# Optimization experiments

Measured on AMD Instinct MI355X. Metric: run time of the kernel, lower is better.

Reference implementation:

```python
import jax, jax.numpy as jnp
import numpy as np

TEMPERATURE = 0.07


def setup_inputs() -> dict:
    key = jax.random.key(0)
    k1, k2 = jax.random.split(key)
    image_tokens = jax.random.normal(k1, (128, 196, 512), dtype=jnp.float32)
    text_tokens = jax.random.normal(k2, (128, 64, 512), dtype=jnp.float32)
    return {"image_tokens": image_tokens, "text_tokens": text_tokens}


def _maxsim(image_tokens, text_tokens):
    # sim[b1, b2, t, i] = <text[b1, t], image[b2, i]>
    sim = jnp.einsum('btd,sid->bsti', text_tokens, image_tokens)  # [B, B, T, I]
    sim_max = jnp.max(sim, axis=-1)        # max over image tokens -> [B, B, T]
    return jnp.mean(sim_max, axis=-1)      # mean over text tokens -> [B, B]


def _cross_entropy_diag(logits):
    # CE against targets = arange(B): mean(logsumexp(row) - row[b, b])
    lse = jax.nn.logsumexp(logits, axis=-1)
    diag = jnp.diagonal(logits)
    return jnp.mean(lse - diag)


def reference(image_tokens, text_tokens):
    sim = _maxsim(image_tokens, text_tokens)
    logits = sim / TEMPERATURE
    loss_i2t = _cross_entropy_diag(logits)
    loss_t2i = _cross_entropy_diag(logits.T)
    return (loss_i2t + loss_t2i) * 0.5
```

## Files before the change

### kernel.cpp

```cpp
#include <hip/hip_runtime.h>
#include <stdint.h>


typedef __attribute__((ext_vector_type(4))) int i4v;

#define BB 128
#define TT 64
#define II 196
#define IP 208
#define DD 512
#define BKK 64
#define KSTEPS (DD / BKK)

static __device__ __forceinline__ void async16(const void* g, void* l) {
  __builtin_amdgcn_global_load_lds(
      (const __attribute__((address_space(1))) void*)g,
      (__attribute__((address_space(3))) void*)l, 16, 0, 0);
}

static __device__ __forceinline__ unsigned q8(float x) {
  float r = rintf(x * 32.0f);
  r = fmaxf(-127.0f, fminf(127.0f, r));
  return (unsigned)((int)r) & 255u;
}

static __device__ __forceinline__ unsigned pk4(float a, float b, float c, float d) {
  return q8(a) | (q8(b) << 8) | (q8(c) << 16) | (q8(d) << 24);
}

#define TEXT_BLOCKS 1024
#define IMG_BLOCKS  3328
__global__ void pack_k(const float* __restrict__ img, const float* __restrict__ txt,
                       uint4* __restrict__ imgq, uint4* __restrict__ txtq) {
  uint4 o;
  if (blockIdx.x < TEXT_BLOCKS) {
    int c = blockIdx.x * 256 + threadIdx.x;
    const float4* in4 = (const float4*)txt;
    float4 f0 = in4[4 * c], f1 = in4[4 * c + 1], f2 = in4[4 * c + 2], f3 = in4[4 * c + 3];
    o.x = pk4(f0.x, f0.y, f0.z, f0.w);
    o.y = pk4(f1.x, f1.y, f1.z, f1.w);
    o.z = pk4(f2.x, f2.y, f2.z, f2.w);
    o.w = pk4(f3.x, f3.y, f3.z, f3.w);
    txtq[c] = o;
  } else {
    int c = (blockIdx.x - TEXT_BLOCKS) * 256 + threadIdx.x;
    int e = c * 16;
    int k = e & (DD - 1);
    int tok = e >> 9;
    int b2 = tok / IP;
    int r = tok - b2 * IP;
    if (r < II) {
      const float4* in4 = (const float4*)(img + ((size_t)(b2 * II + r) * DD + k));
      float4 f0 = in4[0], f1 = in4[1], f2 = in4[2], f3 = in4[3];
      o.x = pk4(f0.x, f0.y, f0.z, f0.w);
      o.y = pk4(f1.x, f1.y, f1.z, f1.w);
      o.z = pk4(f2.x, f2.y, f2.z, f2.w);
      o.w = pk4(f3.x, f3.y, f3.z, f3.w);
    } else {
      o = make_uint4(0u, 0u, 0u, 0u);
    }
    imgq[c] = o;
  }
}

__global__ __launch_bounds__(256, 2) void maxsim_gemm_k(
    const char* __restrict__ A,
    const char* __restrict__ Bm,
    float* __restrict__ sim)
{
  __shared__ __align__(16) char As0[128 * BKK], As1[128 * BKK];
  __shared__ __align__(16) char Bs0[IP * BKK],  Bs1[IP * BKK];
  __shared__ int partial[2][128];

  const int pr  = blockIdx.x;
  const int b2  = blockIdx.y;
  const int tid = threadIdx.x;
  const int w = tid >> 6, l = tid & 63;
  const int m = l & 15, q = l >> 4;
  const int waveM = w >> 1;
  const int waveN = w & 1;
  const int nt = 7 - waveN;

  const int ca0 = tid, ca1 = tid + 256;
  const int cb0 = tid, cb1 = tid + 256, cb2 = tid + 512, cb3 = 768 + l;
#define AOFF(c) ((unsigned)((pr * 128 + ((c) >> 2)) * DD + ((((c) & 3) ^ ((((c) >> 2) >> 1) & 3)) * 16)))
#define BOFF(c) ((unsigned)((b2 * IP + ((c) >> 2)) * DD + ((((c) & 3) ^ ((((c) >> 2) >> 1) & 3)) * 16)))
  const unsigned oA0 = AOFF(ca0), oA1 = AOFF(ca1);
  const unsigned oB0 = BOFF(cb0), oB1 = BOFF(cb1), oB2 = BOFF(cb2), oB3 = BOFF(cb3);

#define ISSUE(AS, BS, k0) do {                                    \
    async16(A  + oA0 + (k0), (char*)(AS) + ca0 * 16);             \
    async16(A  + oA1 + (k0), (char*)(AS) + ca1 * 16);             \
    async16(Bm + oB0 + (k0), (char*)(BS) + cb0 * 16);             \
    async16(Bm + oB1 + (k0), (char*)(BS) + cb1 * 16);             \
    async16(Bm + oB2 + (k0), (char*)(BS) + cb2 * 16);             \
    if (w == 0) async16(Bm + oB3 + (k0), (char*)(BS) + cb3 * 16); \
  } while (0)

  i4v acc[4][7];
#pragma unroll
  for (int mi = 0; mi < 4; ++mi)
#pragma unroll
    for (int nj = 0; nj < 7; ++nj)
      acc[mi][nj] = (i4v){0, 0, 0, 0};

  const int swz = q ^ ((m >> 1) & 3);

#define COMPUTE(AS, BS) do {                                               \
    const i4v* Av = (const i4v*)(AS);                                      \
    const i4v* Bv = (const i4v*)(BS);                                      \
    i4v af[4];                                                             \
    _Pragma("unroll")                                                      \
    for (int mi = 0; mi < 4; ++mi)                                         \
      af[mi] = Av[(waveM * 64 + mi * 16 + m) * 4 + swz];                   \
    _Pragma("unroll")                                                      \
    for (int nj = 0; nj < 7; ++nj) {                                       \
      if (nj < nt) {                                                       \
        i4v bf = Bv[(waveN * 112 + nj * 16 + m) * 4 + swz];                \
        _Pragma("unroll")                                                  \
        for (int mi = 0; mi < 4; ++mi)                                     \
          acc[mi][nj] = __builtin_amdgcn_mfma_i32_16x16x64_i8(             \
              af[mi], bf, acc[mi][nj], 0, 0, 0);                           \
      }                                                                    \
    }                                                                      \
  } while (0)

  ISSUE(As0, Bs0, 0);
  __syncthreads();
  for (int ks = 0; ks < KSTEPS; ks += 2) {
    ISSUE(As1, Bs1, (ks + 1) * BKK);
    COMPUTE(As0, Bs0);
    __syncthreads();
    if (ks + 2 < KSTEPS) ISSUE(As0, Bs0, (ks + 2) * BKK);
    COMPUTE(As1, Bs1);
    __syncthreads();
  }

  const int NEG = -(1 << 30);
#pragma unroll
  for (int mi = 0; mi < 4; ++mi) {
    int v0 = NEG, v1 = NEG, v2 = NEG, v3 = NEG;
#pragma unroll
    for (int nj = 0; nj < 7; ++nj) {
      if (nj < nt) {
        int col = waveN * 112 + nj * 16 + m;
        bool valid = col < II;
        v0 = max(v0, valid ? acc[mi][nj][0] : NEG);
        v1 = max(v1, valid ? acc[mi][nj][1] : NEG);
        v2 = max(v2, valid ? acc[mi][nj][2] : NEG);
        v3 = max(v3, valid ? acc[mi][nj][3] : NEG);
      }
    }
#pragma unroll
    for (int off = 1; off < 16; off <<= 1) {
      v0 = max(v0, __shfl_xor(v0, off));
      v1 = max(v1, __shfl_xor(v1, off));
      v2 = max(v2, __shfl_xor(v2, off));
      v3 = max(v3, __shfl_xor(v3, off));
    }
    if (m == 0) {
      int rowb = waveM * 64 + mi * 16 + q * 4;
      partial[waveN][rowb + 0] = v0;
      partial[waveN][rowb + 1] = v1;
      partial[waveN][rowb + 2] = v2;
      partial[waveN][rowb + 3] = v3;
    }
  }
  __syncthreads();

  if (tid < 128) {
    int v = max(partial[0][tid], partial[1][tid]);
#pragma unroll
    for (int off = 1; off < 64; off <<= 1) v += __shfl_xor(v, off);
    if ((tid & 63) == 0) {
      int b1 = pr * 2 + (tid >> 6);
      sim[b1 * BB + b2] = (float)v * (1.0f / 65536.0f);
    }
  }
}

#define LSTR 132
__global__ void loss_k(const float* __restrict__ sim, float* __restrict__ out) {
  __shared__ float S[BB * LSTR];
  __shared__ float red[4];
  const int tid = threadIdx.x;
#pragma unroll
  for (int i = 0; i < 16; ++i) {
    int c = tid + 256 * i;
    int r = c >> 5, col4 = c & 31;
    float4 v = ((const float4*)sim)[c];
    *(float4*)&S[r * LSTR + col4 * 4] = v;
  }
  __syncthreads();

  const int b = tid & 127;
  const bool rowmode = tid < 128;
  const float sc = 1.0f / 0.07f;
  float mx = -3.0e38f;
  for (int j = 0; j < BB; ++j) {
    float v = rowmode ? S[b * LSTR + j] : S[j * LSTR + b];
    mx = fmaxf(mx, v);
  }
  float s = 0.f;
  for (int j = 0; j < BB; ++j) {
    float v = rowmode ? S[b * LSTR + j] : S[j * LSTR + b];
    s += __expf((v - mx) * sc);
  }
  float d = S[b * LSTR + b];
  float v = (mx - d) * sc + __logf(s);
#pragma unroll
  for (int off = 1; off < 64; off <<= 1) v += __shfl_xor(v, off);
  if ((tid & 63) == 0) red[tid >> 6] = v;
  __syncthreads();
  if (tid == 0) out[0] = (red[0] + red[1] + red[2] + red[3]) * 0.5f / 128.0f;
}

extern "C" void kernel_launch(void* const* d_in, const int* in_sizes, int n_in,
                              void* d_out, int out_size, void* d_ws, size_t ws_size,
                              hipStream_t stream) {
  const float* img = (const float*)d_in[0];
  const float* txt = (const float*)d_in[1];
  float* out = (float*)d_out;

  char* ws = (char*)d_ws;
  const size_t TXT_Q = (size_t)BB * TT * DD;
  const size_t IMG_Q = (size_t)BB * IP * DD;
  char* txtq = ws;
  char* imgq = ws + TXT_Q;
  float* sim = (float*)(ws + TXT_Q + IMG_Q);

  pack_k<<<TEXT_BLOCKS + IMG_BLOCKS, 256, 0, stream>>>(img, txt, (uint4*)imgq, (uint4*)txtq);
  maxsim_gemm_k<<<dim3(64, 128), 256, 0, stream>>>(txtq, imgq, sim);
  loss_k<<<1, 256, 0, stream>>>(sim, out);
}
```

Before: 227.7 us.

## Make GEMM persistent over image batches and fuse loss via last-block counter

Each of 512 blocks now loops over 16 image batches for a fixed text tile. The next batch's first K-slice is prefetched while the current batch finishes, so the tile pipeline carries across batches instead of restarting per block. The MFMA work is rebalanced so the 13th N-tile is split between the two waves and no padded-column tiles are computed. The separate loss kernel is folded in: the last block, found through an atomic counter, does the loss, at the cost of an extra memset and threadfences.

```diff
diff --git a/kernel.cpp b/kernel.cpp
--- a/kernel.cpp
+++ b/kernel.cpp
@@ -10,7 +10,8 @@
 #define IP 208
 #define DD 512
 #define BKK 64
-#define KSTEPS (DD / BKK)
+#define NTASK 16
+#define LSTR 132
 
 static __device__ __forceinline__ void async16(const void* g, void* l) {
   __builtin_amdgcn_global_load_lds(
@@ -23,7 +24,6 @@
   r = fmaxf(-127.0f, fminf(127.0f, r));
   return (unsigned)((int)r) & 255u;
 }
-
 static __device__ __forceinline__ unsigned pk4(float a, float b, float c, float d) {
   return q8(a) | (q8(b) << 8) | (q8(c) << 16) | (q8(d) << 24);
 }
@@ -66,43 +66,53 @@
 __global__ __launch_bounds__(256, 2) void maxsim_gemm_k(
     const char* __restrict__ A,
     const char* __restrict__ Bm,
-    float* __restrict__ sim)
+    float* __restrict__ sim,
+    int* __restrict__ counter,
+    float* __restrict__ out)
 {
-  __shared__ __align__(16) char As0[128 * BKK], As1[128 * BKK];
-  __shared__ __align__(16) char Bs0[IP * BKK],  Bs1[IP * BKK];
-  __shared__ int partial[2][128];
-
-  const int pr  = blockIdx.x;
-  const int b2  = blockIdx.y;
+  __shared__ __align__(16) char smem[BB * LSTR * 4];
+  char* As0 = smem;
+  char* As1 = smem + 8192;
+  char* Bs0 = smem + 16384;
+  char* Bs1 = smem + 29696;
+  int*  partial = (int*)(smem + 43008);
+  __shared__ float red[4];
+  __shared__ int lastflag;
+
+  const int j   = blockIdx.x;
+  const int pr  = j >> 3;
+  const int b2_0 = j & 7;
   const int tid = threadIdx.x;
   const int w = tid >> 6, l = tid & 63;
   const int m = l & 15, q = l >> 4;
   const int waveM = w >> 1;
   const int waveN = w & 1;
-  const int nt = 7 - waveN;
 
   const int ca0 = tid, ca1 = tid + 256;
   const int cb0 = tid, cb1 = tid + 256, cb2 = tid + 512, cb3 = 768 + l;
 #define AOFF(c) ((unsigned)((pr * 128 + ((c) >> 2)) * DD + ((((c) & 3) ^ ((((c) >> 2) >> 1) & 3)) * 16)))
-#define BOFF(c) ((unsigned)((b2 * IP + ((c) >> 2)) * DD + ((((c) & 3) ^ ((((c) >> 2) >> 1) & 3)) * 16)))
+#define BOFF(c) ((unsigned)((b2_0 * IP + ((c) >> 2)) * DD + ((((c) & 3) ^ ((((c) >> 2) >> 1) & 3)) * 16)))
   const unsigned oA0 = AOFF(ca0), oA1 = AOFF(ca1);
   const unsigned oB0 = BOFF(cb0), oB1 = BOFF(cb1), oB2 = BOFF(cb2), oB3 = BOFF(cb3);
-
-#define ISSUE(AS, BS, k0) do {                                    \
-    async16(A  + oA0 + (k0), (char*)(AS) + ca0 * 16);             \
-    async16(A  + oA1 + (k0), (char*)(AS) + ca1 * 16);             \
-    async16(Bm + oB0 + (k0), (char*)(BS) + cb0 * 16);             \
-    async16(Bm + oB1 + (k0), (char*)(BS) + cb1 * 16);             \
-    async16(Bm + oB2 + (k0), (char*)(BS) + cb2 * 16);             \
-    if (w == 0) async16(Bm + oB3 + (k0), (char*)(BS) + cb3 * 16); \
+  const unsigned BSTR = 8u * IP * DD;
+
+#define ISSUE(AS, BS, k0, bo_) do {                                      \
+    async16(A  + oA0 + (k0), (AS) + ca0 * 16);                           \
+    async16(A  + oA1 + (k0), (AS) + ca1 * 16);                           \
+    async16(Bm + oB0 + (bo_) + (k0), (BS) + cb0 * 16);                   \
+    async16(Bm + oB1 + (bo_) + (k0), (BS) + cb1 * 16);                   \
+    async16(Bm + oB2 + (bo_) + (k0), (BS) + cb2 * 16);                   \
+    if (w == 0) async16(Bm + oB3 + (bo_) + (k0), (BS) + cb3 * 16);       \
   } while (0)
 
-  i4v acc[4][7];
+  i4v am[4][6], a12[2];
 #pragma unroll
   for (int mi = 0; mi < 4; ++mi)
 #pragma unroll
-    for (int nj = 0; nj < 7; ++nj)
-      acc[mi][nj] = (i4v){0, 0, 0, 0};
+    for (int nj = 0; nj < 6; ++nj)
+      am[mi][nj] = (i4v){0, 0, 0, 0};
+  a12[0] = (i4v){0, 0, 0, 0};
+  a12[1] = (i4v){0, 0, 0, 0};
 
   const int swz = q ^ ((m >> 1) & 3);
 
@@ -114,76 +124,105 @@
     for (int mi = 0; mi < 4; ++mi)                                         \
       af[mi] = Av[(waveM * 64 + mi * 16 + m) * 4 + swz];                   \
     _Pragma("unroll")                                                      \
-    for (int nj = 0; nj < 7; ++nj) {                                       \
-      if (nj < nt) {                                                       \
-        i4v bf = Bv[(waveN * 112 + nj * 16 + m) * 4 + swz];                \
-        _Pragma("unroll")                                                  \
-        for (int mi = 0; mi < 4; ++mi)                                     \
-          acc[mi][nj] = __builtin_amdgcn_mfma_i32_16x16x64_i8(             \
-              af[mi], bf, acc[mi][nj], 0, 0, 0);                           \
+    for (int nj = 0; nj < 6; ++nj) {                                       \
+      i4v bf = Bv[((waveN * 6 + nj) * 16 + m) * 4 + swz];                  \
+      _Pragma("unroll")                                                    \
+      for (int mi = 0; mi < 4; ++mi)                                       \
+        am[mi][nj] = __builtin_amdgcn_mfma_i32_16x16x64_i8(                \
+            af[mi], bf, am[mi][nj], 0, 0, 0);                              \
+    }                                                                      \
+    {                                                                      \
+      i4v bf = Bv[(192 + m) * 4 + swz];                                    \
+      if (waveN == 0) {                                                    \
+        a12[0] = __builtin_amdgcn_mfma_i32_16x16x64_i8(af[0], bf, a12[0], 0, 0, 0); \
+        a12[1] = __builtin_amdgcn_mfma_i32_16x16x64_i8(af[1], bf, a12[1], 0, 0, 0); \
+      } else {                                                             \
+        a12[0] = __builtin_amdgcn_mfma_i32_16x16x64_i8(af[2], bf, a12[0], 0, 0, 0); \
+        a12[1] = __builtin_amdgcn_mfma_i32_16x16x64_i8(af[3], bf, a12[1], 0, 0, 0); \
       }                                                                    \
     }                                                                      \
   } while (0)
 
-  ISSUE(As0, Bs0, 0);
-  __syncthreads();
-  for (int ks = 0; ks < KSTEPS; ks += 2) {
-    ISSUE(As1, Bs1, (ks + 1) * BKK);
-    COMPUTE(As0, Bs0);
+  unsigned bo = 0;
+  ISSUE(As0, Bs0, 0, 0);
+  __syncthreads();
+
+#pragma unroll 1
+  for (int t = 0; t < NTASK; ++t) {
+    for (int ks = 0; ks < 8; ks += 2) {
+      ISSUE(As1, Bs1, (ks + 1) * BKK, bo);
+      COMPUTE(As0, Bs0);
+      __syncthreads();
+      if (ks + 2 < 8)            ISSUE(As0, Bs0, (ks + 2) * BKK, bo);
+      else if (t + 1 < NTASK)    ISSUE(As0, Bs0, 0, bo + BSTR);
+      COMPUTE(As1, Bs1);
+      __syncthreads();
+    }
+
+    const int NEG = -(1 << 30);
+#pragma unroll
+    for (int mi = 0; mi < 4; ++mi) {
+      int v0 = NEG, v1 = NEG, v2 = NEG, v3 = NEG;
+#pragma unroll
+      for (int nj = 0; nj < 6; ++nj) {
+        v0 = max(v0, am[mi][nj][0]);
+        v1 = max(v1, am[mi][nj][1]);
+        v2 = max(v2, am[mi][nj][2]);
+        v3 = max(v3, am[mi][nj][3]);
+      }
+      if ((mi >> 1) == waveN) {
+        int z = mi & 1;
+        bool valid = m < 4;
+        v0 = max(v0, valid ? a12[z][0] : NEG);
+        v1 = max(v1, valid ? a12[z][1] : NEG);
+        v2 = max(v2, valid ? a12[z][2] : NEG);
+        v3 = max(v3, valid ? a12[z][3] : NEG);
+      }
+#pragma unroll
+      for (int off = 1; off < 16; off <<= 1) {
+        v0 = max(v0, __shfl_xor(v0, off));
+        v1 = max(v1, __shfl_xor(v1, off));
+        v2 = max(v2, __shfl_xor(v2, off));
+        v3 = max(v3, __shfl_xor(v3, off));
+      }
+      if (m == 0) {
+        int rowb = waveM * 64 + mi * 16 + q * 4;
+        partial[waveN * 128 + rowb + 0] = v0;
+        partial[waveN * 128 + rowb + 1] = v1;
+        partial[waveN * 128 + rowb + 2] = v2;
+        partial[waveN * 128 + rowb + 3] = v3;
+      }
+    }
     __syncthreads();
-    if (ks + 2 < KSTEPS) ISSUE(As0, Bs0, (ks + 2) * BKK);
-    COMPUTE(As1, Bs1);
+
+    if (tid < 128) {
+      int v = max(partial[tid], partial[128 + tid]);
+#pragma unroll
+      for (int off = 1; off < 64; off <<= 1) v += __shfl_xor(v, off);
+      if ((tid & 63) == 0) {
+        int b1 = pr * 2 + (tid >> 6);
+        sim[b1 * BB + (b2_0 + 8 * t)] = (float)v * (1.0f / 65536.0f);
+      }
+    }
     __syncthreads();
-  }
-
-  const int NEG = -(1 << 30);
-#pragma unroll
-  for (int mi = 0; mi < 4; ++mi) {
-    int v0 = NEG, v1 = NEG, v2 = NEG, v3 = NEG;
-#pragma unroll
-    for (int nj = 0; nj < 7; ++nj) {
-      if (nj < nt) {
-        int col = waveN * 112 + nj * 16 + m;
-        bool valid = col < II;
-        v0 = max(v0, valid ? acc[mi][nj][0] : NEG);
-        v1 = max(v1, valid ? acc[mi][nj][1] : NEG);
-        v2 = max(v2, valid ? acc[mi][nj][2] : NEG);
-        v3 = max(v3, valid ? acc[mi][nj][3] : NEG);
-      }
-    }
-#pragma unroll
-    for (int off = 1; off < 16; off <<= 1) {
-      v0 = max(v0, __shfl_xor(v0, off));
-      v1 = max(v1, __shfl_xor(v1, off));
-      v2 = max(v2, __shfl_xor(v2, off));
-      v3 = max(v3, __shfl_xor(v3, off));
-    }
-    if (m == 0) {
-      int rowb = waveM * 64 + mi * 16 + q * 4;
-      partial[waveN][rowb + 0] = v0;
-      partial[waveN][rowb + 1] = v1;
-      partial[waveN][rowb + 2] = v2;
-      partial[waveN][rowb + 3] = v3;
-    }
-  }
-  __syncthreads();
-
-  if (tid < 128) {
-    int v = max(partial[0][tid], partial[1][tid]);
-#pragma unroll
-    for (int off = 1; off < 64; off <<= 1) v += __shfl_xor(v, off);
-    if ((tid & 63) == 0) {
-      int b1 = pr * 2 + (tid >> 6);
-      sim[b1 * BB + b2] = (float)v * (1.0f / 65536.0f);
-    }
-  }
-}
-
-#define LSTR 132
-__global__ void loss_k(const float* __restrict__ sim, float* __restrict__ out) {
-  __shared__ float S[BB * LSTR];
-  __shared__ float red[4];
-  const int tid = threadIdx.x;
+
+#pragma unroll
+    for (int mi = 0; mi < 4; ++mi)
+#pragma unroll
+      for (int nj = 0; nj < 6; ++nj)
+        am[mi][nj] = (i4v){0, 0, 0, 0};
+    a12[0] = (i4v){0, 0, 0, 0};
+    a12[1] = (i4v){0, 0, 0, 0};
+    bo += BSTR;
+  }
+
+  __threadfence();
+  if (tid == 0) lastflag = (atomicAdd(counter, 1) == 511);
+  __syncthreads();
+  if (!lastflag) return;
+  __threadfence();
+
+  float* S = (float*)smem;
 #pragma unroll
   for (int i = 0; i < 16; ++i) {
     int c = tid + 256 * i;
@@ -197,13 +236,13 @@
   const bool rowmode = tid < 128;
   const float sc = 1.0f / 0.07f;
   float mx = -3.0e38f;
-  for (int j = 0; j < BB; ++j) {
-    float v = rowmode ? S[b * LSTR + j] : S[j * LSTR + b];
+  for (int jj = 0; jj < BB; ++jj) {
+    float v = rowmode ? S[b * LSTR + jj] : S[jj * LSTR + b];
     mx = fmaxf(mx, v);
   }
   float s = 0.f;
-  for (int j = 0; j < BB; ++j) {
-    float v = rowmode ? S[b * LSTR + j] : S[j * LSTR + b];
+  for (int jj = 0; jj < BB; ++jj) {
+    float v = rowmode ? S[b * LSTR + jj] : S[jj * LSTR + b];
     s += __expf((v - mx) * sc);
   }
   float d = S[b * LSTR + b];
@@ -228,8 +267,9 @@
   char* txtq = ws;
   char* imgq = ws + TXT_Q;
   float* sim = (float*)(ws + TXT_Q + IMG_Q);
-
+  int* counter = (int*)(ws + TXT_Q + IMG_Q + 65536);
+
+  hipMemsetAsync(counter, 0, 4, stream);
   pack_k<<<TEXT_BLOCKS + IMG_BLOCKS, 256, 0, stream>>>(img, txt, (uint4*)imgq, (uint4*)txtq);
-  maxsim_gemm_k<<<dim3(64, 128), 256, 0, stream>>>(txtq, imgq, sim);
-  loss_k<<<1, 256, 0, stream>>>(sim, out);
-}
+  maxsim_gemm_k<<<512, 256, 0, stream>>>(txtq, imgq, sim, counter, out);
+}
```

Measured after the change: 267.3 us. +17.4%, slower.

## Shrink GEMM block tile to one text batch per 128-thread block

Applied to the files above, without the earlier changes.

The maxsim GEMM block now covers a single text batch (64 rows) against one image batch, using two waves instead of four. The grid doubles to 128x128 blocks, and each block loads the full image tile for only half as many text rows. This lowers LDS use per block and so may raise occupancy and parallelism. The cost is that image tokens are loaded from global/L2 twice as often overall, and fewer waves per block are left to hide load latency.

```diff
diff --git a/kernel.cpp b/kernel.cpp
--- a/kernel.cpp
+++ b/kernel.cpp
@@ -23,7 +23,6 @@
   r = fmaxf(-127.0f, fminf(127.0f, r));
   return (unsigned)((int)r) & 255u;
 }
-
 static __device__ __forceinline__ unsigned pk4(float a, float b, float c, float d) {
   return q8(a) | (q8(b) << 8) | (q8(c) << 16) | (q8(d) << 24);
 }
@@ -63,30 +62,31 @@
   }
 }
 
-__global__ __launch_bounds__(256, 2) void maxsim_gemm_k(
+__global__ __launch_bounds__(128, 2) void maxsim_gemm_k(
     const char* __restrict__ A,
     const char* __restrict__ Bm,
     float* __restrict__ sim)
 {
-  __shared__ __align__(16) char As0[128 * BKK], As1[128 * BKK];
+  __shared__ __align__(16) char As0[64 * BKK],  As1[64 * BKK];
   __shared__ __align__(16) char Bs0[IP * BKK],  Bs1[IP * BKK];
-  __shared__ int partial[2][128];
-
-  const int pr  = blockIdx.x;
+  __shared__ int partial[2][64];
+
+  const int b1  = blockIdx.x;
   const int b2  = blockIdx.y;
   const int tid = threadIdx.x;
   const int w = tid >> 6, l = tid & 63;
   const int m = l & 15, q = l >> 4;
-  const int waveM = w >> 1;
-  const int waveN = w & 1;
-  const int nt = 7 - waveN;
-
-  const int ca0 = tid, ca1 = tid + 256;
-  const int cb0 = tid, cb1 = tid + 256, cb2 = tid + 512, cb3 = 768 + l;
-#define AOFF(c) ((unsigned)((pr * 128 + ((c) >> 2)) * DD + ((((c) & 3) ^ ((((c) >> 2) >> 1) & 3)) * 16)))
+  const int nt = 7 - w;
+
+  const int ca0 = tid, ca1 = tid + 128;
+  const int cb0 = tid, cb1 = tid + 128, cb2 = tid + 256, cb3 = tid + 384,
+            cb4 = tid + 512, cb5 = tid + 640, cb6 = 768 + l;
+#define AOFF(c) ((unsigned)((b1 * 64 + ((c) >> 2)) * DD + ((((c) & 3) ^ ((((c) >> 2) >> 1) & 3)) * 16)))
 #define BOFF(c) ((unsigned)((b2 * IP + ((c) >> 2)) * DD + ((((c) & 3) ^ ((((c) >> 2) >> 1) & 3)) * 16)))
   const unsigned oA0 = AOFF(ca0), oA1 = AOFF(ca1);
-  const unsigned oB0 = BOFF(cb0), oB1 = BOFF(cb1), oB2 = BOFF(cb2), oB3 = BOFF(cb3);
+  const unsigned oB0 = BOFF(cb0), oB1 = BOFF(cb1), oB2 = BOFF(cb2),
+                 oB3 = BOFF(cb3), oB4 = BOFF(cb4), oB5 = BOFF(cb5),
+                 oB6 = BOFF(cb6);
 
 #define ISSUE(AS, BS, k0) do {                                    \
     async16(A  + oA0 + (k0), (char*)(AS) + ca0 * 16);             \
@@ -94,7 +94,10 @@
     async16(Bm + oB0 + (k0), (char*)(BS) + cb0 * 16);             \
     async16(Bm + oB1 + (k0), (char*)(BS) + cb1 * 16);             \
     async16(Bm + oB2 + (k0), (char*)(BS) + cb2 * 16);             \
-    if (w == 0) async16(Bm + oB3 + (k0), (char*)(BS) + cb3 * 16); \
+    async16(Bm + oB3 + (k0), (char*)(BS) + cb3 * 16);             \
+    async16(Bm + oB4 + (k0), (char*)(BS) + cb4 * 16);             \
+    async16(Bm + oB5 + (k0), (char*)(BS) + cb5 * 16);             \
+    if (w == 0) async16(Bm + oB6 + (k0), (char*)(BS) + cb6 * 16); \
   } while (0)
 
   i4v acc[4][7];
@@ -112,11 +115,11 @@
     i4v af[4];                                                             \
     _Pragma("unroll")                                                      \
     for (int mi = 0; mi < 4; ++mi)                                         \
-      af[mi] = Av[(waveM * 64 + mi * 16 + m) * 4 + swz];                   \
+      af[mi] = Av[(mi * 16 + m) * 4 + swz];                                \
     _Pragma("unroll")                                                      \
     for (int nj = 0; nj < 7; ++nj) {                                       \
       if (nj < nt) {                                                       \
-        i4v bf = Bv[(waveN * 112 + nj * 16 + m) * 4 + swz];                \
+        i4v bf = Bv[(w * 112 + nj * 16 + m) * 4 + swz];                    \
         _Pragma("unroll")                                                  \
         for (int mi = 0; mi < 4; ++mi)                                     \
           acc[mi][nj] = __builtin_amdgcn_mfma_i32_16x16x64_i8(             \
@@ -143,7 +146,7 @@
 #pragma unroll
     for (int nj = 0; nj < 7; ++nj) {
       if (nj < nt) {
-        int col = waveN * 112 + nj * 16 + m;
+        int col = w * 112 + nj * 16 + m;
         bool valid = col < II;
         v0 = max(v0, valid ? acc[mi][nj][0] : NEG);
         v1 = max(v1, valid ? acc[mi][nj][1] : NEG);
@@ -159,23 +162,21 @@
       v3 = max(v3, __shfl_xor(v3, off));
     }
     if (m == 0) {
-      int rowb = waveM * 64 + mi * 16 + q * 4;
-      partial[waveN][rowb + 0] = v0;
-      partial[waveN][rowb + 1] = v1;
-      partial[waveN][rowb + 2] = v2;
-      partial[waveN][rowb + 3] = v3;
-    }
-  }
-  __syncthreads();
-
-  if (tid < 128) {
+      int rowb = mi * 16 + q * 4;
+      partial[w][rowb + 0] = v0;
+      partial[w][rowb + 1] = v1;
+      partial[w][rowb + 2] = v2;
+      partial[w][rowb + 3] = v3;
+    }
+  }
+  __syncthreads();
+
+  if (tid < 64) {
     int v = max(partial[0][tid], partial[1][tid]);
 #pragma unroll
     for (int off = 1; off < 64; off <<= 1) v += __shfl_xor(v, off);
-    if ((tid & 63) == 0) {
-      int b1 = pr * 2 + (tid >> 6);
+    if (tid == 0)
       sim[b1 * BB + b2] = (float)v * (1.0f / 65536.0f);
-    }
   }
 }
 
@@ -230,6 +231,6 @@
   float* sim = (float*)(ws + TXT_Q + IMG_Q);
 
   pack_k<<<TEXT_BLOCKS + IMG_BLOCKS, 256, 0, stream>>>(img, txt, (uint4*)imgq, (uint4*)txtq);
-  maxsim_gemm_k<<<dim3(64, 128), 256, 0, stream>>>(txtq, imgq, sim);
+  maxsim_gemm_k<<<dim3(128, 128), 128, 0, stream>>>(txtq, imgq, sim);
   loss_k<<<1, 256, 0, stream>>>(sim, out);
 }
```

Result: slower. 261.2 us (+14.7%).
